# Optimization experiments

Measured on AMD Instinct MI355X. Metric: run time of the kernel, lower is better.

## Reference

```python
import jax, jax.numpy as jnp
import numpy as np

B, C, D, H, W = 4, 64, 32, 64, 64
S, NH = 8, 4
HD = C // NH


def setup_inputs() -> dict:
    key = jax.random.key(0)
    ks = jax.random.split(key, 8)
    sc = 0.05
    return {
        "x": jax.random.normal(ks[0], (B, C, D, H, W), jnp.float32),
        "slot_init": jax.random.normal(ks[1], (1, C, S), jnp.float32),
        "slot_proj_w": jax.random.normal(ks[2], (C, C), jnp.float32) * sc,
        "slot_proj_b": jnp.zeros((C,), jnp.float32),
        "ln_g": jnp.ones((C,), jnp.float32),
        "ln_b": jnp.zeros((C,), jnp.float32),
        "in_proj_w": jax.random.normal(ks[3], (3 * C, C), jnp.float32) * sc,
        "in_proj_b": jnp.zeros((3 * C,), jnp.float32),
        "out_proj_w": jax.random.normal(ks[4], (C, C), jnp.float32) * sc,
        "out_proj_b": jnp.zeros((C,), jnp.float32),
        "feat_w": jax.random.normal(ks[5], (C, C), jnp.float32) * sc,
        "feat_b": jnp.zeros((C,), jnp.float32),
        "s2f_w": jax.random.normal(ks[6], (C, C), jnp.float32) * sc,
        "s2f_b": jnp.zeros((C,), jnp.float32),
    }


def _l2norm(v, axis):
    # F.normalize: v / max(||v||, eps)
    n = jnp.sqrt(jnp.sum(v * v, axis=axis, keepdims=True))
    return v / jnp.maximum(n, 1e-12)


def reference(x, slot_init, slot_proj_w, slot_proj_b, ln_g, ln_b,
              in_proj_w, in_proj_b, out_proj_w, out_proj_b,
              feat_w, feat_b, s2f_w, s2f_b):
    b, c, d, h, w = x.shape
    n = d * h * w
    x_flat = x.reshape(b, c, n)                                  # (b,c,N)
    slots = jnp.broadcast_to(slot_init, (b, c, S))               # (b,c,S)

    # ---- slot update: cosine-sim cross attention over N ----
    x_norm = _l2norm(x_flat, 1)
    slots_norm = _l2norm(slots, 1)
    sim = jnp.einsum('bcs,bcn->bsn', slots_norm, x_norm)         # (b,S,N)
    attn = jax.nn.softmax(sim, axis=2)
    updates = jnp.einsum('bcn,bsn->bsc', x_flat, attn)           # (b,S,c)
    slots_t = updates @ slot_proj_w.T + slot_proj_b              # (b,S,c)

    # ---- LayerNorm(channels) then tiny MHSA over S=8 slots ----
    mu = jnp.mean(slots_t, axis=-1, keepdims=True)
    var = jnp.mean((slots_t - mu) ** 2, axis=-1, keepdims=True)
    sn = (slots_t - mu) / jnp.sqrt(var + 1e-5) * ln_g + ln_b     # (b,S,c)

    qkv = sn @ in_proj_w.T + in_proj_b                           # (b,S,3c)
    q, k, v = jnp.split(qkv, 3, axis=-1)
    def heads(t):
        return t.reshape(b, S, NH, HD).transpose(0, 2, 1, 3)     # (b,H,S,hd)
    q, k, v = heads(q), heads(k), heads(v)
    scores = jnp.einsum('bhqd,bhkd->bhqk', q, k) / jnp.sqrt(jnp.float32(HD))
    a = jax.nn.softmax(scores, axis=-1)
    o = jnp.einsum('bhqk,bhkd->bhqd', a, v).transpose(0, 2, 1, 3).reshape(b, S, c)
    o = o @ out_proj_w.T + out_proj_b
    slots_t = slots_t + o                                        # (b,S,c)

    # ---- feature broadcast: 1x1x1 conv + slot->feature attention ----
    feat_flat = jnp.einsum('oc,bcn->bon', feat_w, x_flat) + feat_b[None, :, None]
    slots_feat = slots_t @ s2f_w.T + s2f_b                       # (b,S,c)
    sim2 = jnp.einsum('bsc,bcn->bsn', slots_feat, feat_flat)
    attn2 = jax.nn.softmax(sim2, axis=1)                         # softmax over slots
    out = jnp.einsum('bsc,bsn->bcn', slots_t, attn2)             # (b,c,N)
    return out.reshape(b, c, d, h, w) + x
```

## Files before the change

kernel.cpp:

```cpp
#include <hip/hip_runtime.h>
#include <hip/hip_bf16.h>

#define BB   4
#define CC   64
#define SS   8
#define NN   (32*64*64)
#define NH_  4
#define HD_  16
#define TN   256
#define BPB  128

__global__ __launch_bounds__(256) void k_slots_attn(
    const float* __restrict__ x, const float* __restrict__ slot_init,
    float* __restrict__ U_part, float* __restrict__ sume_part)
{
    __shared__ float xt[CC * TN];
    __shared__ float et[SS * TN];
    __shared__ float snT[SS * CC];
    __shared__ float snorm[SS];

    const int tid = threadIdx.x;
    const int b   = blockIdx.x / BPB;
    const int blk = blockIdx.x % BPB;

    if (tid < SS) {
        float ss = 0.f;
        for (int c = 0; c < CC; ++c) { float v = slot_init[c*SS + tid]; ss += v*v; }
        snorm[tid] = fmaxf(sqrtf(ss), 1e-12f);
    }
    __syncthreads();
    if (tid < CC) {
        for (int s = 0; s < SS; ++s) snT[s*CC + tid] = slot_init[tid*SS + s] / snorm[s];
    }
    __syncthreads();

    const int s_own = tid >> 5;
    const int c0    = tid & 31;
    const int c1    = c0 + 32;
    float acc0 = 0.f, acc1 = 0.f, accS = 0.f;

    const float* xb = x + (size_t)b * CC * NN;
    const int ntiles = NN / TN;
    const int wrow = tid >> 6;
    const int j    = tid & 63;

    for (int t = blk; t < ntiles; t += BPB) {
        const int n0 = t * TN;

        #pragma unroll
        for (int k = 0; k < 16; ++k) {
            const int c = k*4 + wrow;
            float4 v = *(const float4*)(xb + (size_t)c * NN + n0 + j*4);
            const int slot = c*64 + (j ^ (c & 7));
            *(float4*)(&xt[slot*4]) = v;
        }
        __syncthreads();

        {
            float ss = 0.f;
            float a[SS];
            #pragma unroll
            for (int s = 0; s < SS; ++s) a[s] = 0.f;
            #pragma unroll
            for (int c4 = 0; c4 < 16; ++c4) {
                float xv[4];
                #pragma unroll
                for (int jj = 0; jj < 4; ++jj) {
                    const int c = c4*4 + jj;
                    xv[jj] = xt[c*TN + (tid ^ ((c & 7) << 2))];
                    ss += xv[jj] * xv[jj];
                }
                #pragma unroll
                for (int s = 0; s < SS; ++s) {
                    float4 g4 = *(const float4*)(&snT[s*CC + c4*4]);
                    a[s] += g4.x*xv[0] + g4.y*xv[1] + g4.z*xv[2] + g4.w*xv[3];
                }
            }
            const float invn = 1.f / fmaxf(sqrtf(ss), 1e-12f);
            #pragma unroll
            for (int s = 0; s < SS; ++s) et[s*TN + tid] = __expf(a[s] * invn);
        }
        __syncthreads();

        #pragma unroll 4
        for (int np4 = 0; np4 < TN/4; ++np4) {
            const float4 e4 = *(const float4*)(&et[s_own*TN + np4*4]);
            const float4 xa = *(const float4*)(&xt[(c0*64 + (np4 ^ (c0 & 7))) * 4]);
            const float4 xc = *(const float4*)(&xt[(c1*64 + (np4 ^ (c1 & 7))) * 4]);
            acc0 += e4.x*xa.x + e4.y*xa.y + e4.z*xa.z + e4.w*xa.w;
            acc1 += e4.x*xc.x + e4.y*xc.y + e4.z*xc.z + e4.w*xc.w;
            accS += e4.x + e4.y + e4.z + e4.w;
        }
        __syncthreads();
    }

    size_t base = (((size_t)b * BPB + blk) * SS + s_own) * CC;
    U_part[base + c0] = acc0;
    U_part[base + c1] = acc1;
    if (c0 == 0)
        sume_part[((size_t)b * BPB + blk) * SS + s_own] = accS;
}

__global__ __launch_bounds__(256) void k_slots_small(
    const float* __restrict__ U_part, const float* __restrict__ sume_part,
    const float* __restrict__ spw, const float* __restrict__ spb,
    const float* __restrict__ lng, const float* __restrict__ lnb,
    const float* __restrict__ ipw, const float* __restrict__ ipb,
    const float* __restrict__ opw, const float* __restrict__ opb,
    const float* __restrict__ s2fw, const float* __restrict__ s2fb,
    const float* __restrict__ fw,  const float* __restrict__ fb,
    float* __restrict__ st_out, float* __restrict__ g_out, float* __restrict__ h_out)
{
    __shared__ float upd[BB*SS*CC];
    __shared__ float st [BB*SS*CC];
    __shared__ float snb[BB*SS*CC];
    __shared__ float qkvs[BB*SS*3*CC];
    __shared__ float ot [BB*SS*CC];
    __shared__ float sfs[BB*SS*CC];
    __shared__ float Ls[BB*SS];

    const int tid  = threadIdx.x;
    const int c    = tid & 63;
    const int quad = tid >> 6;

    float uacc[SS];
    #pragma unroll
    for (int s = 0; s < SS; ++s) uacc[s] = 0.f;
    for (int k = 0; k < BPB; ++k) {
        const float* p = U_part + ((size_t)(quad*BPB + k) * SS) * CC + c;
        #pragma unroll
        for (int s = 0; s < SS; ++s) uacc[s] += p[s*CC];
    }
    if (tid < BB*SS) {
        int b = tid >> 3, s = tid & 7;
        const float* p = sume_part + (size_t)b*BPB*SS + s;
        float acc = 0.f;
        for (int k = 0; k < BPB; ++k) acc += p[k*SS];
        Ls[tid] = acc;
    }
    __syncthreads();
    #pragma unroll
    for (int s = 0; s < SS; ++s)
        upd[(quad*SS + s)*CC + c] = uacc[s] / Ls[quad*SS + s];
    __syncthreads();

    float wreg[CC];

    #pragma unroll
    for (int i = 0; i < 16; ++i)
        *(float4*)&wreg[i*4] = *(const float4*)(spw + c*CC + i*4);
    {
        const float bias = spb[c];
        #pragma unroll
        for (int r = 0; r < SS; ++r) {
            const int bs = quad*SS + r;
            float acc = bias;
            #pragma unroll
            for (int i = 0; i < 16; ++i) {
                float4 u4 = *(const float4*)&upd[bs*CC + i*4];
                acc += u4.x*wreg[i*4+0] + u4.y*wreg[i*4+1]
                     + u4.z*wreg[i*4+2] + u4.w*wreg[i*4+3];
            }
            st[bs*CC + c] = acc;
        }
    }
    __syncthreads();

    {
        const int row = tid >> 3;
        const int l8  = tid & 7;
        float v[8];
        *(float4*)&v[0] = *(const float4*)&st[row*CC + l8*8];
        *(float4*)&v[4] = *(const float4*)&st[row*CC + l8*8 + 4];
        float sum = v[0]+v[1]+v[2]+v[3]+v[4]+v[5]+v[6]+v[7];
        sum += __shfl_xor(sum, 1); sum += __shfl_xor(sum, 2); sum += __shfl_xor(sum, 4);
        const float mu = sum * (1.f/64.f);
        float vs = 0.f;
        #pragma unroll
        for (int jj = 0; jj < 8; ++jj) { float d = v[jj]-mu; vs += d*d; }
        vs += __shfl_xor(vs, 1); vs += __shfl_xor(vs, 2); vs += __shfl_xor(vs, 4);
        const float rstd = rsqrtf(vs*(1.f/64.f) + 1e-5f);
        float4 ga = *(const float4*)(lng + l8*8), gb = *(const float4*)(lng + l8*8 + 4);
        float4 ba = *(const float4*)(lnb + l8*8), bb2 = *(const float4*)(lnb + l8*8 + 4);
        const float gv[8]  = {ga.x,ga.y,ga.z,ga.w,gb.x,gb.y,gb.z,gb.w};
        const float bv[8]  = {ba.x,ba.y,ba.z,ba.w,bb2.x,bb2.y,bb2.z,bb2.w};
        #pragma unroll
        for (int jj = 0; jj < 8; ++jj)
            snb[row*CC + l8*8 + jj] = (v[jj]-mu)*rstd*gv[jj] + bv[jj];
    }
    __syncthreads();

    #pragma unroll 1
    for (int m = 0; m < 3; ++m) {
        #pragma unroll
        for (int i = 0; i < 16; ++i)
            *(float4*)&wreg[i*4] = *(const float4*)(ipw + (size_t)(m*CC + c)*CC + i*4);
        const float bias = ipb[m*CC + c];
        #pragma unroll
        for (int r = 0; r < SS; ++r) {
            const int bs = quad*SS + r;
            float acc = bias;
            #pragma unroll
            for (int i = 0; i < 16; ++i) {
                float4 u4 = *(const float4*)&snb[bs*CC + i*4];
                acc += u4.x*wreg[i*4+0] + u4.y*wreg[i*4+1]
                     + u4.z*wreg[i*4+2] + u4.w*wreg[i*4+3];
            }
            qkvs[bs*3*CC + m*CC + c] = acc;
        }
    }
    __syncthreads();

    if (tid < BB*NH_*SS) {
        const int b = tid >> 5, h = (tid >> 3) & 3, q = tid & 7;
        const float* base = &qkvs[b*SS*3*CC];
        float qreg[HD_];
        #pragma unroll
        for (int i = 0; i < 4; ++i)
            *(float4*)&qreg[i*4] = *(const float4*)&base[q*3*CC + h*HD_ + i*4];
        float srow[SS];
        float m = -1e30f;
        #pragma unroll
        for (int k = 0; k < SS; ++k) {
            float kreg[HD_];
            #pragma unroll
            for (int i = 0; i < 4; ++i)
                *(float4*)&kreg[i*4] = *(const float4*)&base[k*3*CC + CC + h*HD_ + i*4];
            float acc = 0.f;
            #pragma unroll
            for (int d = 0; d < HD_; ++d) acc += qreg[d]*kreg[d];
            srow[k] = acc * 0.25f;
            m = fmaxf(m, srow[k]);
        }
        float l = 0.f;
        #pragma unroll
        for (int k = 0; k < SS; ++k) { srow[k] = __expf(srow[k]-m); l += srow[k]; }
        const float inv = 1.f / l;
        float oreg[HD_];
        #pragma unroll
        for (int d = 0; d < HD_; ++d) oreg[d] = 0.f;
        #pragma unroll
        for (int k = 0; k < SS; ++k) {
            float vreg[HD_];
            #pragma unroll
            for (int i = 0; i < 4; ++i)
                *(float4*)&vreg[i*4] = *(const float4*)&base[k*3*CC + 2*CC + h*HD_ + i*4];
            #pragma unroll
            for (int d = 0; d < HD_; ++d) oreg[d] += srow[k]*vreg[d];
        }
        #pragma unroll
        for (int d = 0; d < HD_; ++d)
            ot[(b*SS + q)*CC + h*HD_ + d] = oreg[d] * inv;
    }
    __syncthreads();

    #pragma unroll
    for (int i = 0; i < 16; ++i)
        *(float4*)&wreg[i*4] = *(const float4*)(opw + c*CC + i*4);
    {
        const float bias = opb[c];
        #pragma unroll
        for (int r = 0; r < SS; ++r) {
            const int bs = quad*SS + r;
            float acc = bias;
            #pragma unroll
            for (int i = 0; i < 16; ++i) {
                float4 u4 = *(const float4*)&ot[bs*CC + i*4];
                acc += u4.x*wreg[i*4+0] + u4.y*wreg[i*4+1]
                     + u4.z*wreg[i*4+2] + u4.w*wreg[i*4+3];
            }
            st[bs*CC + c] += acc;
        }
    }
    __syncthreads();

    #pragma unroll
    for (int i = 0; i < 16; ++i)
        *(float4*)&wreg[i*4] = *(const float4*)(s2fw + c*CC + i*4);
    {
        const float bias = s2fb[c];
        #pragma unroll
        for (int r = 0; r < SS; ++r) {
            const int bs = quad*SS + r;
            float acc = bias;
            #pragma unroll
            for (int i = 0; i < 16; ++i) {
                float4 u4 = *(const float4*)&st[bs*CC + i*4];
                acc += u4.x*wreg[i*4+0] + u4.y*wreg[i*4+1]
                     + u4.z*wreg[i*4+2] + u4.w*wreg[i*4+3];
            }
            sfs[bs*CC + c] = acc;
            st_out[bs*CC + c] = st[bs*CC + c];
        }
    }
    __syncthreads();

    #pragma unroll
    for (int o = 0; o < CC; ++o) wreg[o] = fw[o*CC + c];
    #pragma unroll
    for (int r = 0; r < SS; ++r) {
        const int bs = quad*SS + r;
        float acc = 0.f;
        #pragma unroll
        for (int i = 0; i < 16; ++i) {
            float4 u4 = *(const float4*)&sfs[bs*CC + i*4];
            acc += u4.x*wreg[i*4+0] + u4.y*wreg[i*4+1]
                 + u4.z*wreg[i*4+2] + u4.w*wreg[i*4+3];
        }
        g_out[bs*CC + c] = acc;
    }
    if (tid < BB*SS) {
        const float* p = &sfs[tid * CC];
        float acc = 0.f;
        for (int o = 0; o < CC; ++o) acc += p[o] * fb[o];
        h_out[tid] = acc;
    }
}

__global__ __launch_bounds__(256) void k_feat(
    const float* __restrict__ x,
    const float* __restrict__ st_g, const float* __restrict__ g_g,
    const float* __restrict__ h_g,
    float* __restrict__ out)
{
    __shared__ float stS[SS*CC];
    __shared__ float gS [SS*CC];
    __shared__ float hS [SS];

    const int tid = threadIdx.x;
    const int b  = blockIdx.x >> 9;
    const int n  = ((blockIdx.x & 511) << 8) + tid;

    for (int i = tid; i < SS*CC; i += 256) {
        stS[i] = st_g[b*SS*CC + i];
        gS[i]  = g_g [b*SS*CC + i];
    }
    if (tid < SS) hS[tid] = h_g[b*SS + tid];
    __syncthreads();

    const float* xb = x + (size_t)b * CC * NN + n;
    float xc[CC];
    #pragma unroll
    for (int c = 0; c < CC; ++c) xc[c] = xb[(size_t)c * NN];

    float a[SS];
    #pragma unroll
    for (int s = 0; s < SS; ++s) a[s] = hS[s];
    #pragma unroll
    for (int c4 = 0; c4 < CC/4; ++c4) {
        #pragma unroll
        for (int s = 0; s < SS; ++s) {
            float4 g4 = *(const float4*)(&gS[s*CC + c4*4]);
            a[s] += g4.x*xc[c4*4+0] + g4.y*xc[c4*4+1]
                  + g4.z*xc[c4*4+2] + g4.w*xc[c4*4+3];
        }
    }

    float m = a[0];
    #pragma unroll
    for (int s = 1; s < SS; ++s) m = fmaxf(m, a[s]);
    float l = 0.f;
    #pragma unroll
    for (int s = 0; s < SS; ++s) { a[s] = __expf(a[s] - m); l += a[s]; }
    const float inv = 1.f / l;

    float* ob = out + (size_t)b * CC * NN + n;
    #pragma unroll
    for (int c4 = 0; c4 < CC/4; ++c4) {
        float o0 = 0.f, o1 = 0.f, o2 = 0.f, o3 = 0.f;
        #pragma unroll
        for (int s = 0; s < SS; ++s) {
            float4 s4 = *(const float4*)(&stS[s*CC + c4*4]);
            o0 += s4.x * a[s]; o1 += s4.y * a[s];
            o2 += s4.z * a[s]; o3 += s4.w * a[s];
        }
        ob[(size_t)(c4*4+0) * NN] = o0 * inv + xc[c4*4+0];
        ob[(size_t)(c4*4+1) * NN] = o1 * inv + xc[c4*4+1];
        ob[(size_t)(c4*4+2) * NN] = o2 * inv + xc[c4*4+2];
        ob[(size_t)(c4*4+3) * NN] = o3 * inv + xc[c4*4+3];
    }
}

extern "C" void kernel_launch(void* const* d_in, const int* in_sizes, int n_in,
                              void* d_out, int out_size, void* d_ws, size_t ws_size,
                              hipStream_t stream) {
    const float* x         = (const float*)d_in[0];
    const float* slot_init = (const float*)d_in[1];
    const float* spw       = (const float*)d_in[2];
    const float* spb       = (const float*)d_in[3];
    const float* lng       = (const float*)d_in[4];
    const float* lnb       = (const float*)d_in[5];
    const float* ipw       = (const float*)d_in[6];
    const float* ipb       = (const float*)d_in[7];
    const float* opw       = (const float*)d_in[8];
    const float* opb       = (const float*)d_in[9];
    const float* fw        = (const float*)d_in[10];
    const float* fb        = (const float*)d_in[11];
    const float* s2fw      = (const float*)d_in[12];
    const float* s2fb      = (const float*)d_in[13];
    float* out = (float*)d_out;

    float* w         = (float*)d_ws;
    float* U_part    = w;
    float* sume_part = w + 262144;
    float* st_out    = w + 266240;
    float* g_out     = w + 268288;
    float* h_out     = w + 270336;

    k_slots_attn<<<BB * BPB, 256, 0, stream>>>(x, slot_init, U_part, sume_part);
    k_slots_small<<<1, 256, 0, stream>>>(U_part, sume_part, spw, spb, lng, lnb,
                                         ipw, ipb, opw, opb, s2fw, s2fb,
                                         fw, fb, st_out, g_out, h_out);
    k_feat<<<BB * (NN/256), 256, 0, stream>>>(x, st_out, g_out, h_out, out);
}
```

Baseline: 153.9 us.

## Parallelize slot-small stage across batches and fold s2f/feat weights into one matrix

Splits the single-block slot reduction into a 32-block partial-sum reduction kernel, then runs the small slot MLP/attention with one block per batch instead of one block for all batches. A separate precompute kernel multiplies s2f and feat weights into one matrix M plus bias vectors, collapsing two chained 64x64 projections into one. The aim is to cut the serial latency of the one-block bottleneck between the two large x-streaming kernels. In exchange it adds two more kernel launches, and the weight fold slightly reorders floating-point accumulation.

```diff
diff --git a/kernel.cpp b/kernel.cpp
--- a/kernel.cpp
+++ b/kernel.cpp
@@ -101,156 +101,191 @@
         sume_part[((size_t)b * BPB + blk) * SS + s_own] = accS;
 }
 
+__global__ __launch_bounds__(256) void k_precomp(
+    const float* __restrict__ s2fw, const float* __restrict__ s2fb,
+    const float* __restrict__ fw, const float* __restrict__ fb,
+    float* __restrict__ M, float* __restrict__ g0v,
+    float* __restrict__ hv, float* __restrict__ h0)
+{
+    const int tid = threadIdx.x;
+    if (blockIdx.x < 16) {
+        const int cp = blockIdx.x*4 + (tid >> 6);
+        const int c  = tid & 63;
+        float acc = 0.f;
+        #pragma unroll 8
+        for (int o = 0; o < CC; ++o)
+            acc += s2fw[o*CC + cp] * fw[o*CC + c];
+        M[cp*CC + c] = acc;
+    } else {
+        if (tid < 64) {
+            float acc = 0.f;
+            #pragma unroll 8
+            for (int o = 0; o < CC; ++o) acc += s2fb[o] * fw[o*CC + tid];
+            g0v[tid] = acc;
+        } else if (tid < 128) {
+            const int cp = tid - 64;
+            float acc = 0.f;
+            #pragma unroll 8
+            for (int o = 0; o < CC; ++o) acc += s2fw[o*CC + cp] * fb[o];
+            hv[cp] = acc;
+        } else if (tid == 128) {
+            float acc = 0.f;
+            for (int o = 0; o < CC; ++o) acc += s2fb[o] * fb[o];
+            *h0 = acc;
+        }
+    }
+}
+
+__global__ __launch_bounds__(256) void k_reduce2(
+    const float* __restrict__ U_part, const float* __restrict__ sume_part,
+    float* __restrict__ upd_g)
+{
+    __shared__ float part[4][64];
+    __shared__ float lbuf[128];
+    __shared__ float Lsh;
+    const int tid = threadIdx.x;
+    const int b = blockIdx.x >> 3, s = blockIdx.x & 7;
+    const int c = tid & 63, kc = tid >> 6;
+
+    float lv = 0.f;
+    if (tid < 128) lv = sume_part[(size_t)(b*BPB + tid)*SS + s];
+
+    float acc = 0.f;
+    const float* base = U_part + ((size_t)(b*BPB + kc*32)*SS + s)*CC + c;
+    #pragma unroll 8
+    for (int k = 0; k < 32; ++k)
+        acc += base[(size_t)k * SS * CC];
+    part[kc][c] = acc;
+    if (tid < 128) lbuf[tid] = lv;
+    __syncthreads();
+
+    if (tid < 64) {
+        float v = lbuf[tid] + lbuf[tid + 64];
+        v += __shfl_xor(v, 1); v += __shfl_xor(v, 2); v += __shfl_xor(v, 4);
+        v += __shfl_xor(v, 8); v += __shfl_xor(v, 16); v += __shfl_xor(v, 32);
+        if (tid == 0) Lsh = v;
+    }
+    __syncthreads();
+
+    if (tid < 64) {
+        float u = part[0][c] + part[1][c] + part[2][c] + part[3][c];
+        upd_g[((size_t)b*SS + s)*CC + c] = u / Lsh;
+    }
+}
+
 __global__ __launch_bounds__(256) void k_slots_small(
-    const float* __restrict__ U_part, const float* __restrict__ sume_part,
+    const float* __restrict__ upd_g,
     const float* __restrict__ spw, const float* __restrict__ spb,
     const float* __restrict__ lng, const float* __restrict__ lnb,
     const float* __restrict__ ipw, const float* __restrict__ ipb,
     const float* __restrict__ opw, const float* __restrict__ opb,
-    const float* __restrict__ s2fw, const float* __restrict__ s2fb,
-    const float* __restrict__ fw,  const float* __restrict__ fb,
+    const float* __restrict__ M, const float* __restrict__ g0v,
+    const float* __restrict__ hv, const float* __restrict__ h0,
     float* __restrict__ st_out, float* __restrict__ g_out, float* __restrict__ h_out)
 {
-    __shared__ float upd[BB*SS*CC];
-    __shared__ float st [BB*SS*CC];
-    __shared__ float snb[BB*SS*CC];
-    __shared__ float qkvs[BB*SS*3*CC];
-    __shared__ float ot [BB*SS*CC];
-    __shared__ float sfs[BB*SS*CC];
-    __shared__ float Ls[BB*SS];
+    __shared__ float upd[SS*CC];
+    __shared__ float st [SS*CC];
+    __shared__ float snb[SS*CC];
+    __shared__ float qkv[SS*3*CC];
+    __shared__ float ot [SS*CC];
 
     const int tid  = threadIdx.x;
+    const int b    = blockIdx.x;
     const int c    = tid & 63;
     const int quad = tid >> 6;
-
-    float uacc[SS];
-    #pragma unroll
-    for (int s = 0; s < SS; ++s) uacc[s] = 0.f;
-    for (int k = 0; k < BPB; ++k) {
-        const float* p = U_part + ((size_t)(quad*BPB + k) * SS) * CC + c;
-        #pragma unroll
-        for (int s = 0; s < SS; ++s) uacc[s] += p[s*CC];
-    }
-    if (tid < BB*SS) {
-        int b = tid >> 3, s = tid & 7;
-        const float* p = sume_part + (size_t)b*BPB*SS + s;
-        float acc = 0.f;
-        for (int k = 0; k < BPB; ++k) acc += p[k*SS];
-        Ls[tid] = acc;
-    }
-    __syncthreads();
-    #pragma unroll
-    for (int s = 0; s < SS; ++s)
-        upd[(quad*SS + s)*CC + c] = uacc[s] / Ls[quad*SS + s];
-    __syncthreads();
-
+    const int r0 = quad*2, r1 = r0 + 1;
     float wreg[CC];
 
     #pragma unroll
     for (int i = 0; i < 16; ++i)
         *(float4*)&wreg[i*4] = *(const float4*)(spw + c*CC + i*4);
+    upd[r0*CC + c] = upd_g[(b*SS + r0)*CC + c];
+    upd[r1*CC + c] = upd_g[(b*SS + r1)*CC + c];
+    __syncthreads();
+
     {
         const float bias = spb[c];
-        #pragma unroll
-        for (int r = 0; r < SS; ++r) {
-            const int bs = quad*SS + r;
-            float acc = bias;
-            #pragma unroll
-            for (int i = 0; i < 16; ++i) {
-                float4 u4 = *(const float4*)&upd[bs*CC + i*4];
-                acc += u4.x*wreg[i*4+0] + u4.y*wreg[i*4+1]
-                     + u4.z*wreg[i*4+2] + u4.w*wreg[i*4+3];
-            }
-            st[bs*CC + c] = acc;
-        }
+        float a0 = bias, a1 = bias;
+        #pragma unroll
+        for (int i = 0; i < 16; ++i) {
+            float4 u0 = *(const float4*)&upd[r0*CC + i*4];
+            float4 u1 = *(const float4*)&upd[r1*CC + i*4];
+            a0 += u0.x*wreg[i*4+0] + u0.y*wreg[i*4+1] + u0.z*wreg[i*4+2] + u0.w*wreg[i*4+3];
+            a1 += u1.x*wreg[i*4+0] + u1.y*wreg[i*4+1] + u1.z*wreg[i*4+2] + u1.w*wreg[i*4+3];
+        }
+        st[r0*CC + c] = a0;
+        st[r1*CC + c] = a1;
     }
     __syncthreads();
 
     {
-        const int row = tid >> 3;
-        const int l8  = tid & 7;
-        float v[8];
-        *(float4*)&v[0] = *(const float4*)&st[row*CC + l8*8];
-        *(float4*)&v[4] = *(const float4*)&st[row*CC + l8*8 + 4];
-        float sum = v[0]+v[1]+v[2]+v[3]+v[4]+v[5]+v[6]+v[7];
+        const int row = tid >> 5, l = tid & 31;
+        float v0 = st[row*CC + l], v1 = st[row*CC + l + 32];
+        float sum = v0 + v1;
         sum += __shfl_xor(sum, 1); sum += __shfl_xor(sum, 2); sum += __shfl_xor(sum, 4);
+        sum += __shfl_xor(sum, 8); sum += __shfl_xor(sum, 16);
         const float mu = sum * (1.f/64.f);
-        float vs = 0.f;
-        #pragma unroll
-        for (int jj = 0; jj < 8; ++jj) { float d = v[jj]-mu; vs += d*d; }
+        const float d0 = v0 - mu, d1 = v1 - mu;
+        float vs = d0*d0 + d1*d1;
         vs += __shfl_xor(vs, 1); vs += __shfl_xor(vs, 2); vs += __shfl_xor(vs, 4);
-        const float rstd = rsqrtf(vs*(1.f/64.f) + 1e-5f);
-        float4 ga = *(const float4*)(lng + l8*8), gb = *(const float4*)(lng + l8*8 + 4);
-        float4 ba = *(const float4*)(lnb + l8*8), bb2 = *(const float4*)(lnb + l8*8 + 4);
-        const float gv[8]  = {ga.x,ga.y,ga.z,ga.w,gb.x,gb.y,gb.z,gb.w};
-        const float bv[8]  = {ba.x,ba.y,ba.z,ba.w,bb2.x,bb2.y,bb2.z,bb2.w};
-        #pragma unroll
-        for (int jj = 0; jj < 8; ++jj)
-            snb[row*CC + l8*8 + jj] = (v[jj]-mu)*rstd*gv[jj] + bv[jj];
-    }
-    __syncthreads();
-
-    #pragma unroll 1
+        vs += __shfl_xor(vs, 8); vs += __shfl_xor(vs, 16);
+        const float rstd = rsqrtf(vs * (1.f/64.f) + 1e-5f);
+        snb[row*CC + l]      = d0 * rstd * lng[l]      + lnb[l];
+        snb[row*CC + l + 32] = d1 * rstd * lng[l + 32] + lnb[l + 32];
+    }
+    __syncthreads();
+
     for (int m = 0; m < 3; ++m) {
         #pragma unroll
         for (int i = 0; i < 16; ++i)
             *(float4*)&wreg[i*4] = *(const float4*)(ipw + (size_t)(m*CC + c)*CC + i*4);
         const float bias = ipb[m*CC + c];
-        #pragma unroll
-        for (int r = 0; r < SS; ++r) {
-            const int bs = quad*SS + r;
-            float acc = bias;
-            #pragma unroll
-            for (int i = 0; i < 16; ++i) {
-                float4 u4 = *(const float4*)&snb[bs*CC + i*4];
-                acc += u4.x*wreg[i*4+0] + u4.y*wreg[i*4+1]
-                     + u4.z*wreg[i*4+2] + u4.w*wreg[i*4+3];
-            }
-            qkvs[bs*3*CC + m*CC + c] = acc;
-        }
-    }
-    __syncthreads();
-
-    if (tid < BB*NH_*SS) {
-        const int b = tid >> 5, h = (tid >> 3) & 3, q = tid & 7;
-        const float* base = &qkvs[b*SS*3*CC];
+        float a0 = bias, a1 = bias;
+        #pragma unroll
+        for (int i = 0; i < 16; ++i) {
+            float4 u0 = *(const float4*)&snb[r0*CC + i*4];
+            float4 u1 = *(const float4*)&snb[r1*CC + i*4];
+            a0 += u0.x*wreg[i*4+0] + u0.y*wreg[i*4+1] + u0.z*wreg[i*4+2] + u0.w*wreg[i*4+3];
+            a1 += u1.x*wreg[i*4+0] + u1.y*wreg[i*4+1] + u1.z*wreg[i*4+2] + u1.w*wreg[i*4+3];
+        }
+        qkv[r0*3*CC + m*CC + c] = a0;
+        qkv[r1*3*CC + m*CC + c] = a1;
+    }
+    __syncthreads();
+
+    if (tid < NH_*SS) {
+        const int h = tid >> 3, q = tid & 7;
         float qreg[HD_];
         #pragma unroll
         for (int i = 0; i < 4; ++i)
-            *(float4*)&qreg[i*4] = *(const float4*)&base[q*3*CC + h*HD_ + i*4];
+            *(float4*)&qreg[i*4] = *(const float4*)&qkv[q*3*CC + h*HD_ + i*4];
         float srow[SS];
-        float m = -1e30f;
+        float mx = -1e30f;
         #pragma unroll
         for (int k = 0; k < SS; ++k) {
-            float kreg[HD_];
-            #pragma unroll
-            for (int i = 0; i < 4; ++i)
-                *(float4*)&kreg[i*4] = *(const float4*)&base[k*3*CC + CC + h*HD_ + i*4];
             float acc = 0.f;
             #pragma unroll
-            for (int d = 0; d < HD_; ++d) acc += qreg[d]*kreg[d];
+            for (int d = 0; d < HD_; ++d)
+                acc += qreg[d] * qkv[k*3*CC + CC + h*HD_ + d];
             srow[k] = acc * 0.25f;
-            m = fmaxf(m, srow[k]);
+            mx = fmaxf(mx, srow[k]);
         }
         float l = 0.f;
         #pragma unroll
-        for (int k = 0; k < SS; ++k) { srow[k] = __expf(srow[k]-m); l += srow[k]; }
+        for (int k = 0; k < SS; ++k) { srow[k] = __expf(srow[k] - mx); l += srow[k]; }
         const float inv = 1.f / l;
         float oreg[HD_];
         #pragma unroll
         for (int d = 0; d < HD_; ++d) oreg[d] = 0.f;
         #pragma unroll
         for (int k = 0; k < SS; ++k) {
-            float vreg[HD_];
             #pragma unroll
-            for (int i = 0; i < 4; ++i)
-                *(float4*)&vreg[i*4] = *(const float4*)&base[k*3*CC + 2*CC + h*HD_ + i*4];
-            #pragma unroll
-            for (int d = 0; d < HD_; ++d) oreg[d] += srow[k]*vreg[d];
+            for (int d = 0; d < HD_; ++d)
+                oreg[d] += srow[k] * qkv[k*3*CC + 2*CC + h*HD_ + d];
         }
         #pragma unroll
         for (int d = 0; d < HD_; ++d)
-            ot[(b*SS + q)*CC + h*HD_ + d] = oreg[d] * inv;
+            ot[q*CC + h*HD_ + d] = oreg[d] * inv;
     }
     __syncthreads();
 
@@ -259,61 +294,42 @@
         *(float4*)&wreg[i*4] = *(const float4*)(opw + c*CC + i*4);
     {
         const float bias = opb[c];
-        #pragma unroll
-        for (int r = 0; r < SS; ++r) {
-            const int bs = quad*SS + r;
-            float acc = bias;
-            #pragma unroll
-            for (int i = 0; i < 16; ++i) {
-                float4 u4 = *(const float4*)&ot[bs*CC + i*4];
-                acc += u4.x*wreg[i*4+0] + u4.y*wreg[i*4+1]
-                     + u4.z*wreg[i*4+2] + u4.w*wreg[i*4+3];
-            }
-            st[bs*CC + c] += acc;
-        }
-    }
-    __syncthreads();
-
-    #pragma unroll
-    for (int i = 0; i < 16; ++i)
-        *(float4*)&wreg[i*4] = *(const float4*)(s2fw + c*CC + i*4);
+        float a0 = bias, a1 = bias;
+        #pragma unroll
+        for (int i = 0; i < 16; ++i) {
+            float4 u0 = *(const float4*)&ot[r0*CC + i*4];
+            float4 u1 = *(const float4*)&ot[r1*CC + i*4];
+            a0 += u0.x*wreg[i*4+0] + u0.y*wreg[i*4+1] + u0.z*wreg[i*4+2] + u0.w*wreg[i*4+3];
+            a1 += u1.x*wreg[i*4+0] + u1.y*wreg[i*4+1] + u1.z*wreg[i*4+2] + u1.w*wreg[i*4+3];
+        }
+        st[r0*CC + c] += a0;
+        st[r1*CC + c] += a1;
+    }
+    __syncthreads();
+
+    #pragma unroll 8
+    for (int cp = 0; cp < CC; ++cp) wreg[cp] = M[cp*CC + c];
     {
-        const float bias = s2fb[c];
-        #pragma unroll
-        for (int r = 0; r < SS; ++r) {
-            const int bs = quad*SS + r;
-            float acc = bias;
-            #pragma unroll
-            for (int i = 0; i < 16; ++i) {
-                float4 u4 = *(const float4*)&st[bs*CC + i*4];
-                acc += u4.x*wreg[i*4+0] + u4.y*wreg[i*4+1]
-                     + u4.z*wreg[i*4+2] + u4.w*wreg[i*4+3];
-            }
-            sfs[bs*CC + c] = acc;
-            st_out[bs*CC + c] = st[bs*CC + c];
-        }
-    }
-    __syncthreads();
-
-    #pragma unroll
-    for (int o = 0; o < CC; ++o) wreg[o] = fw[o*CC + c];
-    #pragma unroll
-    for (int r = 0; r < SS; ++r) {
-        const int bs = quad*SS + r;
-        float acc = 0.f;
+        const float g0 = g0v[c];
+        float a0 = g0, a1 = g0;
         #pragma unroll
         for (int i = 0; i < 16; ++i) {
-            float4 u4 = *(const float4*)&sfs[bs*CC + i*4];
-            acc += u4.x*wreg[i*4+0] + u4.y*wreg[i*4+1]
-                 + u4.z*wreg[i*4+2] + u4.w*wreg[i*4+3];
-        }
-        g_out[bs*CC + c] = acc;
-    }
-    if (tid < BB*SS) {
-        const float* p = &sfs[tid * CC];
-        float acc = 0.f;
-        for (int o = 0; o < CC; ++o) acc += p[o] * fb[o];
-        h_out[tid] = acc;
+            float4 s0 = *(const float4*)&st[r0*CC + i*4];
+            float4 s1 = *(const float4*)&st[r1*CC + i*4];
+            a0 += s0.x*wreg[i*4+0] + s0.y*wreg[i*4+1] + s0.z*wreg[i*4+2] + s0.w*wreg[i*4+3];
+            a1 += s1.x*wreg[i*4+0] + s1.y*wreg[i*4+1] + s1.z*wreg[i*4+2] + s1.w*wreg[i*4+3];
+        }
+        g_out[(b*SS + r0)*CC + c] = a0;
+        g_out[(b*SS + r1)*CC + c] = a1;
+        st_out[(b*SS + r0)*CC + c] = st[r0*CC + c];
+        st_out[(b*SS + r1)*CC + c] = st[r1*CC + c];
+    }
+    {
+        const int row = tid >> 5, l = tid & 31;
+        float pv = st[row*CC + l]*hv[l] + st[row*CC + l + 32]*hv[l + 32];
+        pv += __shfl_xor(pv, 1); pv += __shfl_xor(pv, 2); pv += __shfl_xor(pv, 4);
+        pv += __shfl_xor(pv, 8); pv += __shfl_xor(pv, 16);
+        if (l == 0) h_out[b*SS + row] = pv + *h0;
     }
 }
 
@@ -403,13 +419,20 @@
     float* w         = (float*)d_ws;
     float* U_part    = w;
     float* sume_part = w + 262144;
-    float* st_out    = w + 266240;
-    float* g_out     = w + 268288;
-    float* h_out     = w + 270336;
-
+    float* upd_g     = w + 266240;
+    float* Mm        = w + 268288;
+    float* g0v       = w + 272384;
+    float* hv        = w + 272448;
+    float* h0        = w + 272512;
+    float* st_out    = w + 272576;
+    float* g_out     = w + 274624;
+    float* h_out     = w + 276672;
+
+    k_precomp<<<17, 256, 0, stream>>>(s2fw, s2fb, fw, fb, Mm, g0v, hv, h0);
     k_slots_attn<<<BB * BPB, 256, 0, stream>>>(x, slot_init, U_part, sume_part);
-    k_slots_small<<<1, 256, 0, stream>>>(U_part, sume_part, spw, spb, lng, lnb,
-                                         ipw, ipb, opw, opb, s2fw, s2fb,
-                                         fw, fb, st_out, g_out, h_out);
+    k_reduce2<<<BB * SS, 256, 0, stream>>>(U_part, sume_part, upd_g);
+    k_slots_small<<<BB, 256, 0, stream>>>(upd_g, spw, spb, lng, lnb,
+                                          ipw, ipb, opw, opb, Mm, g0v, hv, h0,
+                                          st_out, g_out, h_out);
     k_feat<<<BB * (NN/256), 256, 0, stream>>>(x, st_out, g_out, h_out, out);
 }
```

Result: faster. 139.8 us (-9.1%).
